# Optimization experiments

Hardware: AMD Instinct MI355X
Metric: run time of the kernel (lower is better)

## Reference

```python
import jax, jax.numpy as jnp
import numpy as np
import math

B, T, C, E, H = 16, 256, 6, 512, 8


def setup_inputs() -> dict:
    key = jax.random.key(0)
    ks = jax.random.split(key, 5)
    std = 0.02
    return {
        "x": jax.random.normal(ks[0], (B, T, C, E), dtype=jnp.float32),
        "Wq": jax.random.normal(ks[1], (E, E), dtype=jnp.float32) * std,
        "bq": jnp.zeros((E,), dtype=jnp.float32),
        "Wk": jax.random.normal(ks[2], (E, E), dtype=jnp.float32) * std,
        "bk": jnp.zeros((E,), dtype=jnp.float32),
        "Wv": jax.random.normal(ks[3], (E, E), dtype=jnp.float32) * std,
        "bv": jnp.zeros((E,), dtype=jnp.float32),
        "Wp": jax.random.normal(ks[4], (E, E), dtype=jnp.float32) * std,
        "bp": jnp.zeros((E,), dtype=jnp.float32),
    }


def reference(x, Wq, bq, Wk, bk, Wv, bv, Wp, bp):
    b, t, c, e = x.shape
    hd = e // H
    # nn.Linear: y = x @ W^T + b, then view(B,T,C,H,hd).transpose(1,3) -> (B,H,C,T,hd)
    def heads(W, bias):
        y = jnp.einsum('btce,fe->btcf', x, W) + bias
        return y.reshape(b, t, c, H, hd).transpose(0, 3, 2, 1, 4)  # B,H,C,T,hd

    q = heads(Wq, bq)
    k = heads(Wk, bk)
    v = heads(Wv, bv)

    scale = 1.0 / math.sqrt(hd)
    att = jnp.einsum('bhctd,bhcsd->bhcts', q, k) * scale  # B,H,C,T,T
    causal = jnp.tril(jnp.ones((t, t), dtype=bool))
    att = jnp.where(causal, att, -jnp.inf)
    att = jax.nn.softmax(att, axis=-1)

    y = jnp.einsum('bhcts,bhcsd->bhctd', att, v)  # B,H,C,T,hd
    # permute(0,3,1,2,4) -> (B,T,H,C,hd), then view(B,T,C,E) (faithful to torch)
    y = y.transpose(0, 3, 1, 2, 4).reshape(b, t, c, e)
    return jnp.einsum('btce,fe->btcf', y, Wp) + bp
```

## Files before the change

### kernel.cpp

```cpp
#include <hip/hip_runtime.h>


typedef unsigned short u16;
typedef short bf16x8 __attribute__((ext_vector_type(8)));
typedef float f32x4 __attribute__((ext_vector_type(4)));
typedef u16 u16x4 __attribute__((ext_vector_type(4)));

#define MFMA16(a, b, c) __builtin_amdgcn_mfma_f32_16x16x32_bf16((a), (b), (c), 0, 0, 0)

__device__ __forceinline__ u16 f2b(float f) {
  union { float f; unsigned u; } v; v.f = f;
  unsigned r = v.u + 0x7fffu + ((v.u >> 16) & 1u);
  return (u16)(r >> 16);
}
__device__ __forceinline__ void gl_lds16(const void* g, void* l) {
  __builtin_amdgcn_global_load_lds(
      (const __attribute__((address_space(1))) void*)g,
      (__attribute__((address_space(3))) void*)l, 16, 0, 0);
}

__global__ void cvt_w(const float* W0, const float* W1, const float* W2,
                      const float* W3, u16* dst) {
  const float* src = (blockIdx.y == 0) ? W0 : (blockIdx.y == 1) ? W1
                   : (blockIdx.y == 2) ? W2 : W3;
  const int idx = (blockIdx.x * 256 + threadIdx.x) * 4;
  f32x4 v = *(const f32x4*)(src + idx);
  u16x4 o; o.x = f2b(v.x); o.y = f2b(v.y); o.z = f2b(v.z); o.w = f2b(v.w);
  *(u16x4*)(dst + (size_t)blockIdx.y * 262144 + idx) = o;
}

__global__ void cvt_x(const float* __restrict__ src, u16* __restrict__ dst) {
  const size_t idx = ((size_t)blockIdx.x * 256 + threadIdx.x) * 4;
  f32x4 v = *(const f32x4*)(src + idx);
  u16x4 o; o.x = f2b(v.x); o.y = f2b(v.y); o.z = f2b(v.z); o.w = f2b(v.w);
  *(u16x4*)(dst + idx) = o;
}

__global__ __launch_bounds__(256, 3) void gemm_bt(
    const u16* __restrict__ A,
    const u16* W0, const u16* W1, const u16* W2,
    const float* bs0, const float* bs1, const float* bs2,
    u16* O0, u16* O1, u16* O2, float* OF, int qkv_mode)
{
  const int z = blockIdx.z;
  const u16* W    = (z == 0) ? W0 : (z == 1) ? W1 : W2;
  const float* bs = (z == 0) ? bs0 : (z == 1) ? bs1 : bs2;
  u16* O          = (z == 0) ? O0 : (z == 1) ? O1 : O2;

  const int m0 = (blockIdx.x >> 2) * 128;
  const int n0 = (blockIdx.x & 3) * 128;

  __shared__ u16 As[128 * 64];
  __shared__ u16 Bs[128 * 64];

  const int tid  = threadIdx.x;
  const int lane = tid & 63;
  const int wv   = tid >> 6;
  const int r    = lane & 15;
  const int qd   = lane >> 4;
  const int wm   = (wv & 1) * 64;
  const int wn   = (wv >> 1) * 64;

  f32x4 acc[4][4] = {};

  for (int k0 = 0; k0 < 512; k0 += 64) {
    __syncthreads();
    #pragma unroll
    for (int it = 0; it < 4; ++it) {
      const int idx = it * 256 + tid;
      const int flat = idx * 16;
      const int row  = flat >> 7;
      const int swc  = (flat >> 4) & 7;
      const int gc   = swc ^ (row & 7);
      gl_lds16((const char*)A + (size_t)(m0 + row) * 1024 + k0 * 2 + gc * 16,
               (char*)As + flat);
      gl_lds16((const char*)W + (size_t)(n0 + row) * 1024 + k0 * 2 + gc * 16,
               (char*)Bs + flat);
    }
    __syncthreads();

    #pragma unroll
    for (int ks = 0; ks < 2; ++ks) {
      bf16x8 af[4], bf[4];
      #pragma unroll
      for (int mt = 0; mt < 4; ++mt) {
        const int row = wm + mt * 16 + r;
        const int pch = (ks * 4 + qd) ^ (row & 7);
        af[mt] = *(const bf16x8*)((const char*)As + row * 128 + pch * 16);
      }
      #pragma unroll
      for (int nt = 0; nt < 4; ++nt) {
        const int row = wn + nt * 16 + r;
        const int pch = (ks * 4 + qd) ^ (row & 7);
        bf[nt] = *(const bf16x8*)((const char*)Bs + row * 128 + pch * 16);
      }
      #pragma unroll
      for (int mt = 0; mt < 4; ++mt)
        #pragma unroll
        for (int nt = 0; nt < 4; ++nt)
          acc[mt][nt] = MFMA16(af[mt], bf[nt], acc[mt][nt]);
    }
  }

  float bv[4];
  #pragma unroll
  for (int nt = 0; nt < 4; ++nt) bv[nt] = bs[n0 + wn + nt * 16 + r];

  if (qkv_mode) {
    #pragma unroll
    for (int mt = 0; mt < 4; ++mt) {
      #pragma unroll
      for (int rr = 0; rr < 4; ++rr) {
        const int m   = m0 + wm + mt * 16 + qd * 4 + rr;
        const int b   = m / 1536;
        const int rem = m - b * 1536;
        const int t   = rem / 6;
        const int c   = rem - t * 6;
        #pragma unroll
        for (int nt = 0; nt < 4; ++nt) {
          const int f = n0 + wn + nt * 16 + r;
          const int h = f >> 6;
          const int d = f & 63;
          const size_t addr = ((((size_t)b * 8 + h) * 6 + c) * 256 + t) * 64 + d;
          O[addr] = f2b(acc[mt][nt][rr] + bv[nt]);
        }
      }
    }
  } else {
    #pragma unroll
    for (int mt = 0; mt < 4; ++mt) {
      #pragma unroll
      for (int rr = 0; rr < 4; ++rr) {
        const int m = m0 + wm + mt * 16 + qd * 4 + rr;
        #pragma unroll
        for (int nt = 0; nt < 4; ++nt) {
          const int f = n0 + wn + nt * 16 + r;
          OF[(size_t)m * 512 + f] = acc[mt][nt][rr] + bv[nt];
        }
      }
    }
  }
}

__global__ __launch_bounds__(512, 2) void attn(
    const u16* __restrict__ q_ws, const u16* __restrict__ k_ws,
    const u16* __restrict__ v_ws, u16* __restrict__ y_ws)
{
  const int blk = blockIdx.x;
  const int b   = blk / 48;
  const int h   = (blk / 6) % 8;
  const int c   = blk % 6;
  const size_t base = (size_t)blk * 256 * 64;

  __shared__ u16 Ks[128 * 72];
  __shared__ u16 Vts[64 * 136];
  __shared__ u16 Ps[8][16 * 72];

  const int tid  = threadIdx.x;
  const int lane = tid & 63;
  const int wv   = tid >> 6;
  const int r    = lane & 15;
  const int qd   = lane >> 4;

  const int tiles[2] = { wv, 15 - wv };

  bf16x8 qf[2][2];
  #pragma unroll
  for (int ti = 0; ti < 2; ++ti)
    #pragma unroll
    for (int kc = 0; kc < 2; ++kc)
      qf[ti][kc] = *(const bf16x8*)(q_ws + base +
                     (size_t)(tiles[ti] * 16 + r) * 64 + kc * 32 + qd * 8);

  f32x4 o_acc[2][4] = {};
  float l_acc[2][4] = {{0.f,0.f,0.f,0.f},{0.f,0.f,0.f,0.f}};

  for (int sc = 0; sc < 2; ++sc) {
    __syncthreads();
    #pragma unroll
    for (int it = 0; it < 2; ++it) {
      const int idx = it * 512 + tid;
      const int row = idx >> 3;
      const int c8  = idx & 7;
      *(bf16x8*)(Ks + row * 72 + c8 * 8) =
          *(const bf16x8*)(k_ws + base + (size_t)(sc * 128 + row) * 64 + c8 * 8);
    }
    {
      const int jl = tid & 127;
      const int d0 = (tid >> 7) * 16;
      #pragma unroll
      for (int dd = 0; dd < 16; dd += 8) {
        bf16x8 vv = *(const bf16x8*)(v_ws + base +
                       (size_t)(sc * 128 + jl) * 64 + d0 + dd);
        #pragma unroll
        for (int e = 0; e < 8; ++e)
          Vts[(d0 + dd + e) * 136 + jl] = ((u16*)&vv)[e];
      }
    }
    __syncthreads();

    #pragma unroll
    for (int ti = 0; ti < 2; ++ti) {
      const int mt  = tiles[ti];
      const int i0  = mt * 16;
      const int nch = (mt >> 2) + 1;
      #pragma unroll
      for (int jcl = 0; jcl < 2; ++jcl) {
        const int jc = sc * 2 + jcl;
        if (jc >= nch) continue;
        const int j0l = jcl * 64;
        const int j0g = sc * 128 + j0l;

        f32x4 s[4] = {};
        #pragma unroll
        for (int nt = 0; nt < 4; ++nt)
          #pragma unroll
          for (int kc = 0; kc < 2; ++kc) {
            bf16x8 kf = *(const bf16x8*)(Ks + (j0l + nt * 16 + r) * 72 +
                                         kc * 32 + qd * 8);
            s[nt] = MFMA16(qf[ti][kc], kf, s[nt]);
          }

        #pragma unroll
        for (int nt = 0; nt < 4; ++nt)
          #pragma unroll
          for (int rr = 0; rr < 4; ++rr) {
            const int i = i0 + qd * 4 + rr;
            const int j = j0g + nt * 16 + r;
            float p = __builtin_exp2f(fminf(s[nt][rr], 500.f) *
                                      0.1803368801111244f);
            if (j > i) p = 0.f;
            l_acc[ti][rr] += p;
            Ps[wv][(qd * 4 + rr) * 72 + nt * 16 + r] = f2b(p);
          }
        asm volatile("s_waitcnt lgkmcnt(0)" ::: "memory");

        bf16x8 pf[2];
        #pragma unroll
        for (int kc = 0; kc < 2; ++kc)
          pf[kc] = *(const bf16x8*)(Ps[wv] + r * 72 + kc * 32 + qd * 8);
        #pragma unroll
        for (int ntd = 0; ntd < 4; ++ntd)
          #pragma unroll
          for (int kc = 0; kc < 2; ++kc) {
            bf16x8 vf = *(const bf16x8*)(Vts + (ntd * 16 + r) * 136 +
                                         j0l + kc * 32 + qd * 8);
            o_acc[ti][ntd] = MFMA16(pf[kc], vf, o_acc[ti][ntd]);
          }
      }
    }
  }

  const size_t obase = ((size_t)b * 256) * 3072 + h * 384 + c * 64;
  #pragma unroll
  for (int ti = 0; ti < 2; ++ti) {
    const int i0 = tiles[ti] * 16;
    float linv[4];
    #pragma unroll
    for (int rr = 0; rr < 4; ++rr) {
      float sum = l_acc[ti][rr];
      sum += __shfl_xor(sum, 1, 16);
      sum += __shfl_xor(sum, 2, 16);
      sum += __shfl_xor(sum, 4, 16);
      sum += __shfl_xor(sum, 8, 16);
      linv[rr] = 1.f / sum;
    }
    #pragma unroll
    for (int ntd = 0; ntd < 4; ++ntd)
      #pragma unroll
      for (int rr = 0; rr < 4; ++rr) {
        const int t = i0 + qd * 4 + rr;
        const int d = ntd * 16 + r;
        y_ws[obase + (size_t)t * 3072 + d] = f2b(o_acc[ti][ntd][rr] * linv[rr]);
      }
  }
}

extern "C" void kernel_launch(void* const* d_in, const int* in_sizes, int n_in,
                              void* d_out, int out_size, void* d_ws, size_t ws_size,
                              hipStream_t stream) {
  const float* x  = (const float*)d_in[0];
  const float* Wq = (const float*)d_in[1];
  const float* bq = (const float*)d_in[2];
  const float* Wk = (const float*)d_in[3];
  const float* bk = (const float*)d_in[4];
  const float* Wv = (const float*)d_in[5];
  const float* bv = (const float*)d_in[6];
  const float* Wp = (const float*)d_in[7];
  const float* bp = (const float*)d_in[8];
  float* out = (float*)d_out;

  const size_t PER_B = 256 * 6 * 512;
  const size_t WSEG  = 4 * 262144;

  int NB = 16;
  while (NB > 1 && (WSEG + (size_t)5 * NB * PER_B) * 2 > ws_size) NB >>= 1;

  u16* wbf = (u16*)d_ws;
  u16* Wqb = wbf;
  u16* Wkb = wbf + 262144;
  u16* Wvb = wbf + 2 * 262144;
  u16* Wpb = wbf + 3 * 262144;

  const size_t slab = (size_t)NB * PER_B;
  u16* xbf  = wbf + WSEG;
  u16* q_ws = xbf + slab;
  u16* k_ws = q_ws + slab;
  u16* v_ws = k_ws + slab;
  u16* y_ws = v_ws + slab;

  cvt_w<<<dim3(256, 4), 256, 0, stream>>>(Wq, Wk, Wv, Wp, wbf);

  const int nslab = 16 / NB;
  for (int s = 0; s < nslab; ++s) {
    const float* x_s  = x   + (size_t)s * NB * PER_B;
    float*      out_s = out + (size_t)s * NB * PER_B;
    cvt_x<<<dim3(NB * 768), 256, 0, stream>>>(x_s, xbf);
    gemm_bt<<<dim3(NB * 48, 1, 3), 256, 0, stream>>>(
        xbf, Wqb, Wkb, Wvb, bq, bk, bv, q_ws, k_ws, v_ws, nullptr, 1);
    attn<<<dim3(NB * 48), 512, 0, stream>>>(q_ws, k_ws, v_ws, y_ws);
    gemm_bt<<<dim3(NB * 48, 1, 1), 256, 0, stream>>>(
        y_ws, Wpb, Wpb, Wpb, bp, bp, bp, nullptr, nullptr, nullptr, out_s, 0);
  }
}
```

Measured before the change: 223.2 us.

## Write V transposed from projection GEMM and restructure attention to 4 waves

The QKV projection epilogue now writes V in a transposed (d, t) layout, so the attention kernel reads V fragments straight from global memory and no longer transposes V through shared memory. The attention kernel drops to 256 threads, loads all 256 K rows into LDS once, and has each wave handle four query tiles with balanced causal work. The GEMM grid is remapped to a 2D (m, n) layout. The aim is to remove the scalar LDS transpose and the per-chunk barriers, at the cost of uncoalesced transposed stores in the GEMM epilogue and V loads that now go to global memory.

```diff
diff --git a/kernel.cpp b/kernel.cpp
--- a/kernel.cpp
+++ b/kernel.cpp
@@ -47,8 +47,8 @@
   const float* bs = (z == 0) ? bs0 : (z == 1) ? bs1 : bs2;
   u16* O          = (z == 0) ? O0 : (z == 1) ? O1 : O2;
 
-  const int m0 = (blockIdx.x >> 2) * 128;
-  const int n0 = (blockIdx.x & 3) * 128;
+  const int m0 = blockIdx.x * 128;
+  const int n0 = blockIdx.y * 128;
 
   __shared__ u16 As[128 * 64];
   __shared__ u16 Bs[128 * 64];
@@ -121,7 +121,9 @@
           const int f = n0 + wn + nt * 16 + r;
           const int h = f >> 6;
           const int d = f & 63;
-          const size_t addr = ((((size_t)b * 8 + h) * 6 + c) * 256 + t) * 64 + d;
+          const size_t bhc = ((((size_t)b * 8 + h) * 6 + c) << 14);
+          const size_t addr = bhc + (z == 2 ? (size_t)d * 256 + t
+                                            : (size_t)t * 64 + d);
           O[addr] = f2b(acc[mt][nt][rr] + bv[nt]);
         }
       }
@@ -142,19 +144,18 @@
   }
 }
 
-__global__ __launch_bounds__(512, 2) void attn(
+__global__ __launch_bounds__(256, 3) void attn(
     const u16* __restrict__ q_ws, const u16* __restrict__ k_ws,
-    const u16* __restrict__ v_ws, u16* __restrict__ y_ws)
+    const u16* __restrict__ vt_ws, u16* __restrict__ y_ws)
 {
   const int blk = blockIdx.x;
   const int b   = blk / 48;
   const int h   = (blk / 6) % 8;
   const int c   = blk % 6;
-  const size_t base = (size_t)blk * 256 * 64;
-
-  __shared__ u16 Ks[128 * 72];
-  __shared__ u16 Vts[64 * 136];
-  __shared__ u16 Ps[8][16 * 72];
+  const size_t base = (size_t)blk * 16384;
+
+  __shared__ u16 Ks[256 * 68];
+  __shared__ u16 Ps[4][16 * 68];
 
   const int tid  = threadIdx.x;
   const int lane = tid & 63;
@@ -162,103 +163,84 @@
   const int r    = lane & 15;
   const int qd   = lane >> 4;
 
-  const int tiles[2] = { wv, 15 - wv };
-
-  bf16x8 qf[2][2];
   #pragma unroll
-  for (int ti = 0; ti < 2; ++ti)
+  for (int it = 0; it < 8; ++it) {
+    const int idx = it * 256 + tid;
+    const int row = idx >> 3;
+    const int c8  = idx & 7;
+    *(bf16x8*)(Ks + row * 68 + c8 * 8) =
+        *(const bf16x8*)(k_ws + base + (size_t)row * 64 + c8 * 8);
+  }
+  __syncthreads();
+
+  const size_t obase = ((size_t)b * 256) * 3072 + h * 384 + c * 64;
+
+  #pragma unroll
+  for (int ti = 0; ti < 4; ++ti) {
+    const int mt = (ti == 0) ? wv : (ti == 1) ? (7 - wv)
+                 : (ti == 2) ? (8 + wv) : (15 - wv);
+    const int i0  = mt * 16;
+    const int nch = (mt >> 2) + 1;
+
+    bf16x8 qf[2];
     #pragma unroll
     for (int kc = 0; kc < 2; ++kc)
-      qf[ti][kc] = *(const bf16x8*)(q_ws + base +
-                     (size_t)(tiles[ti] * 16 + r) * 64 + kc * 32 + qd * 8);
-
-  f32x4 o_acc[2][4] = {};
-  float l_acc[2][4] = {{0.f,0.f,0.f,0.f},{0.f,0.f,0.f,0.f}};
-
-  for (int sc = 0; sc < 2; ++sc) {
-    __syncthreads();
-    #pragma unroll
-    for (int it = 0; it < 2; ++it) {
-      const int idx = it * 512 + tid;
-      const int row = idx >> 3;
-      const int c8  = idx & 7;
-      *(bf16x8*)(Ks + row * 72 + c8 * 8) =
-          *(const bf16x8*)(k_ws + base + (size_t)(sc * 128 + row) * 64 + c8 * 8);
-    }
-    {
-      const int jl = tid & 127;
-      const int d0 = (tid >> 7) * 16;
-      #pragma unroll
-      for (int dd = 0; dd < 16; dd += 8) {
-        bf16x8 vv = *(const bf16x8*)(v_ws + base +
-                       (size_t)(sc * 128 + jl) * 64 + d0 + dd);
-        #pragma unroll
-        for (int e = 0; e < 8; ++e)
-          Vts[(d0 + dd + e) * 136 + jl] = ((u16*)&vv)[e];
-      }
-    }
-    __syncthreads();
-
-    #pragma unroll
-    for (int ti = 0; ti < 2; ++ti) {
-      const int mt  = tiles[ti];
-      const int i0  = mt * 16;
-      const int nch = (mt >> 2) + 1;
-      #pragma unroll
-      for (int jcl = 0; jcl < 2; ++jcl) {
-        const int jc = sc * 2 + jcl;
-        if (jc >= nch) continue;
-        const int j0l = jcl * 64;
-        const int j0g = sc * 128 + j0l;
-
-        f32x4 s[4] = {};
-        #pragma unroll
-        for (int nt = 0; nt < 4; ++nt)
-          #pragma unroll
-          for (int kc = 0; kc < 2; ++kc) {
-            bf16x8 kf = *(const bf16x8*)(Ks + (j0l + nt * 16 + r) * 72 +
-                                         kc * 32 + qd * 8);
-            s[nt] = MFMA16(qf[ti][kc], kf, s[nt]);
-          }
-
-        #pragma unroll
-        for (int nt = 0; nt < 4; ++nt)
-          #pragma unroll
-          for (int rr = 0; rr < 4; ++rr) {
-            const int i = i0 + qd * 4 + rr;
-            const int j = j0g + nt * 16 + r;
-            float p = __builtin_exp2f(fminf(s[nt][rr], 500.f) *
-                                      0.1803368801111244f);
-            if (j > i) p = 0.f;
-            l_acc[ti][rr] += p;
-            Ps[wv][(qd * 4 + rr) * 72 + nt * 16 + r] = f2b(p);
-          }
-        asm volatile("s_waitcnt lgkmcnt(0)" ::: "memory");
-
-        bf16x8 pf[2];
+      qf[kc] = *(const bf16x8*)(q_ws + base + (size_t)(i0 + r) * 64 +
+                                kc * 32 + qd * 8);
+
+    f32x4 o_acc[4] = {};
+    float l_acc[4] = {0.f, 0.f, 0.f, 0.f};
+
+    for (int jc = 0; jc < nch; ++jc) {
+      const int j0 = jc * 64;
+
+      bf16x8 vf[4][2];
+      #pragma unroll
+      for (int ntd = 0; ntd < 4; ++ntd)
         #pragma unroll
         for (int kc = 0; kc < 2; ++kc)
-          pf[kc] = *(const bf16x8*)(Ps[wv] + r * 72 + kc * 32 + qd * 8);
-        #pragma unroll
-        for (int ntd = 0; ntd < 4; ++ntd)
-          #pragma unroll
-          for (int kc = 0; kc < 2; ++kc) {
-            bf16x8 vf = *(const bf16x8*)(Vts + (ntd * 16 + r) * 136 +
-                                         j0l + kc * 32 + qd * 8);
-            o_acc[ti][ntd] = MFMA16(pf[kc], vf, o_acc[ti][ntd]);
-          }
-      }
-    }
-  }
-
-  const size_t obase = ((size_t)b * 256) * 3072 + h * 384 + c * 64;
-  #pragma unroll
-  for (int ti = 0; ti < 2; ++ti) {
-    const int i0 = tiles[ti] * 16;
+          vf[ntd][kc] = *(const bf16x8*)(vt_ws + base +
+                          (size_t)(ntd * 16 + r) * 256 + j0 + kc * 32 + qd * 8);
+
+      f32x4 s[4] = {};
+      #pragma unroll
+      for (int nt = 0; nt < 4; ++nt)
+        #pragma unroll
+        for (int kc = 0; kc < 2; ++kc) {
+          bf16x8 kf = *(const bf16x8*)(Ks + (j0 + nt * 16 + r) * 68 +
+                                       kc * 32 + qd * 8);
+          s[nt] = MFMA16(qf[kc], kf, s[nt]);
+        }
+
+      #pragma unroll
+      for (int nt = 0; nt < 4; ++nt)
+        #pragma unroll
+        for (int rr = 0; rr < 4; ++rr) {
+          const int i = i0 + qd * 4 + rr;
+          const int j = j0 + nt * 16 + r;
+          float p = __builtin_exp2f(fminf(s[nt][rr], 500.f) *
+                                    0.1803368801111244f);
+          if (j > i) p = 0.f;
+          l_acc[rr] += p;
+          Ps[wv][(qd * 4 + rr) * 68 + nt * 16 + r] = f2b(p);
+        }
+      asm volatile("s_waitcnt lgkmcnt(0)" ::: "memory");
+
+      bf16x8 pf[2];
+      #pragma unroll
+      for (int kc = 0; kc < 2; ++kc)
+        pf[kc] = *(const bf16x8*)(Ps[wv] + r * 68 + kc * 32 + qd * 8);
+      #pragma unroll
+      for (int ntd = 0; ntd < 4; ++ntd)
+        #pragma unroll
+        for (int kc = 0; kc < 2; ++kc)
+          o_acc[ntd] = MFMA16(pf[kc], vf[ntd][kc], o_acc[ntd]);
+    }
+
     float linv[4];
     #pragma unroll
     for (int rr = 0; rr < 4; ++rr) {
-      float sum = l_acc[ti][rr];
+      float sum = l_acc[rr];
       sum += __shfl_xor(sum, 1, 16);
       sum += __shfl_xor(sum, 2, 16);
       sum += __shfl_xor(sum, 4, 16);
@@ -271,7 +253,7 @@
       for (int rr = 0; rr < 4; ++rr) {
         const int t = i0 + qd * 4 + rr;
         const int d = ntd * 16 + r;
-        y_ws[obase + (size_t)t * 3072 + d] = f2b(o_acc[ti][ntd][rr] * linv[rr]);
+        y_ws[obase + (size_t)t * 3072 + d] = f2b(o_acc[ntd][rr] * linv[rr]);
       }
   }
 }
@@ -306,8 +288,8 @@
   u16* xbf  = wbf + WSEG;
   u16* q_ws = xbf + slab;
   u16* k_ws = q_ws + slab;
-  u16* v_ws = k_ws + slab;
-  u16* y_ws = v_ws + slab;
+  u16* vt_ws = k_ws + slab;
+  u16* y_ws = vt_ws + slab;
 
   cvt_w<<<dim3(256, 4), 256, 0, stream>>>(Wq, Wk, Wv, Wp, wbf);
 
@@ -316,10 +298,10 @@
     const float* x_s  = x   + (size_t)s * NB * PER_B;
     float*      out_s = out + (size_t)s * NB * PER_B;
     cvt_x<<<dim3(NB * 768), 256, 0, stream>>>(x_s, xbf);
-    gemm_bt<<<dim3(NB * 48, 1, 3), 256, 0, stream>>>(
-        xbf, Wqb, Wkb, Wvb, bq, bk, bv, q_ws, k_ws, v_ws, nullptr, 1);
-    attn<<<dim3(NB * 48), 512, 0, stream>>>(q_ws, k_ws, v_ws, y_ws);
-    gemm_bt<<<dim3(NB * 48, 1, 1), 256, 0, stream>>>(
+    gemm_bt<<<dim3(NB * 12, 4, 3), 256, 0, stream>>>(
+        xbf, Wqb, Wkb, Wvb, bq, bk, bv, q_ws, k_ws, vt_ws, nullptr, 1);
+    attn<<<dim3(NB * 48), 256, 0, stream>>>(q_ws, k_ws, vt_ws, y_ws);
+    gemm_bt<<<dim3(NB * 12, 4, 1), 256, 0, stream>>>(
         y_ws, Wpb, Wpb, Wpb, bp, bp, bp, nullptr, nullptr, nullptr, out_s, 0);
   }
 }
```

Measured after the change: 278.3 us. 24.7% more time.
